# Performance work log

Measured on AMD Instinct MI355X. Metric: run time of the kernel, lower is better.

Reference implementation:

```python
import jax, jax.numpy as jnp
from jax import lax
import numpy as np

GAMMA = 1.0
BIG = 1e10  # stand-in for +inf; exp(-BIG/gamma) underflows to 0 and keeps grads finite


def pairwise_sq_euclidean(A, B):
    # A: (B,T1,K), B: (B,T2,K) -> (B,T1,T2); 0.5*||a-b||^2 expanded to avoid (B,T1,T2,K)
    aa = 0.5 * jnp.sum(A * A, axis=-1)  # (B,T1)
    bb = 0.5 * jnp.sum(B * B, axis=-1)  # (B,T2)
    ab = jnp.einsum('bik,bjk->bij', A, B)
    return aa[:, :, None] + bb[:, None, :] - ab


def soft_dtw(C, gamma):
    # C: (B, m, n). Sequential DP: V[i,j] = C[i-1,j-1] + softmin_gamma(V[i,j-1], V[i-1,j-1], V[i-1,j])
    Bsz, m, n = C.shape
    dt = C.dtype
    big = jnp.asarray(BIG, dt)
    # row 0 of V: V[0,0]=0, V[0,j]=inf
    v0 = jnp.concatenate([jnp.zeros((Bsz, 1), dt), jnp.full((Bsz, n), big, dt)], axis=1)

    def row_step(v_prev, c_row):
        # v_prev: (B, n+1) = V[i-1, :]; c_row: (B, n) = C[:, i-1, :]
        def col_step(v_left, inp):
            c, v_diag, v_up = inp  # each (B,)
            prev = jnp.stack([v_left, v_diag, v_up], axis=-1)  # (B,3)
            minv = -gamma * jax.nn.logsumexp(-prev / gamma, axis=-1)
            v_new = c + minv
            return v_new, v_new

        xs = (c_row.T, v_prev[:, :-1].T, v_prev[:, 1:].T)  # (n, B) each
        _, vals = lax.scan(col_step, jnp.full((Bsz,), big, dt), xs)
        v_row = jnp.concatenate([jnp.full((Bsz, 1), big, dt), vals.T], axis=1)
        return v_row, None

    v_final, _ = lax.scan(row_step, v0, jnp.moveaxis(C, 1, 0))
    return v_final[:, -1]  # (B,)


def setup_inputs() -> dict:
    key = jax.random.key(0)
    k1, k2 = jax.random.split(key)
    X = jax.random.normal(k1, (512, 256, 64), dtype=jnp.float32)
    Y = jax.random.normal(k2, (512, 256, 64), dtype=jnp.float32)
    return {"X": X, "Y": Y}


def reference(X, Y):
    gamma = jnp.asarray(GAMMA, X.dtype)
    s_xy = soft_dtw(pairwise_sq_euclidean(X, Y), gamma)
    s_xx = soft_dtw(pairwise_sq_euclidean(X, X), gamma)
    s_yy = soft_dtw(pairwise_sq_euclidean(Y, Y), gamma)
    D = s_xy - 0.5 * s_xx - 0.5 * s_yy
    # normalize=False, reduction='mean'
    return jnp.mean(D)
```

## Files before the change

kernel.cpp:

```cpp
#include <hip/hip_runtime.h>

typedef _Float16 h8 __attribute__((ext_vector_type(8)));
typedef float f4 __attribute__((ext_vector_type(4)));

#define TT 256
#define KK 64
#define LOG2E 1.44269504f
#define LN2 0.69314718f
#define RL 32
#define RSTR 65
#define DEADD (1 << 28)

__global__ __launch_bounds__(64, 2)
void sdtw_fused3(const float* __restrict__ X, const float* __restrict__ Y,
                 float* __restrict__ out) {
  const int p = blockIdx.x;
  const int type = p >> 9;
  const int b = p & 511;
  const float* Ap = (type == 2 ? Y : X) + (size_t)b * TT * KK;
  const float* Bp = (type == 1 ? X : Y) + (size_t)b * TT * KK;
  const float wgt = (type == 0) ? (LN2 / 512.0f) : (-LN2 / 1024.0f);

  __shared__ unsigned int ring0[RL * RSTR];
  __shared__ unsigned int ring1[RL * RSTR];
  __shared__ float saa[TT];
  __shared__ float sbb[TT];

  const int t = threadIdx.x;
  const int hk = t >> 4, lr = t & 15;

  #pragma unroll
  for (int i = 0; i < 33; ++i) {
    int idx = i * 64 + t;
    if (idx < RL * RSTR) { ring0[idx] = 0u; ring1[idx] = 0u; }
  }

  h8 af[16][2];
  #pragma unroll
  for (int Rt = 0; Rt < 16; ++Rt) {
    float s = 0.f;
    #pragma unroll
    for (int kk = 0; kk < 2; ++kk) {
      const float4* src = (const float4*)(Ap + (Rt * 16 + lr) * KK + kk * 32 + hk * 8);
      float4 x = src[0], y = src[1];
      af[Rt][kk] = (h8){(_Float16)x.x, (_Float16)x.y, (_Float16)x.z, (_Float16)x.w,
                        (_Float16)y.x, (_Float16)y.y, (_Float16)y.z, (_Float16)y.w};
      s += x.x * x.x + x.y * x.y + x.z * x.z + x.w * x.w
         + y.x * y.x + y.y * y.y + y.z * y.z + y.w * y.w;
    }
    s += __shfl_xor(s, 16);
    s += __shfl_xor(s, 32);
    if (hk == (Rt & 3)) saa[Rt * 16 + lr] = 0.5f * LOG2E * s;
  }

  h8 bwin[4][2];

  float E1 = 0.f, E2 = 0.f, E3 = 0.f, E4 = 0.f;
  int d1 = DEADD, d2 = DEADD, d3 = DEADD, d4 = DEADD;
  float dgE = (t == 0) ? 1.0f : 0.f;
  int dgd = (t == 0) ? 0 : DEADD;

  auto cell = [&](float& vE, int& vd, float EL, int dL, float ED, int dD,
                  float EU, int dU, float m, int ci) {
    int ref = min(min(dL, dD), dU);
    float S = ldexpf(EL, ref - dL) + ldexpf(ED, ref - dD) + ldexpf(EU, ref - dU);
    float v = m * S;
    unsigned int u = __builtin_bit_cast(unsigned int, v);
    vE = __builtin_bit_cast(float, (u & 0x007FFFFFu) | 0x3F000000u);
    vd = ref + ci + 126 - (int)(u >> 23);
  };

  auto step = [&](unsigned int w0, unsigned int w1) {
    float upE = __shfl_up(E4, 1);
    int upd = __shfl_up(d4, 1);
    if (t == 0) { upE = 0.f; upd = DEADD; }
    float m0 = __builtin_amdgcn_cvt_f32_fp8((int)w0, 0);
    float m1 = __builtin_amdgcn_cvt_f32_fp8((int)w0, 1);
    float m2 = __builtin_amdgcn_cvt_f32_fp8((int)w0, 2);
    float m3 = __builtin_amdgcn_cvt_f32_fp8((int)w0, 3);
    int ci0 = (int)(w1 & 255u), ci1 = (int)((w1 >> 8) & 255u);
    int ci2 = (int)((w1 >> 16) & 255u), ci3 = (int)(w1 >> 24);
    float v1E, v2E, v3E, v4E; int v1d, v2d, v3d, v4d;
    cell(v1E, v1d, E1, d1, dgE, dgd, upE, upd, m0, ci0);
    cell(v2E, v2d, E2, d2, E1, d1, v1E, v1d, m1, ci1);
    cell(v3E, v3d, E3, d3, E2, d2, v2E, v2d, m2, ci2);
    cell(v4E, v4d, E4, d4, E3, d3, v3E, v3d, m3, ci3);
    E1 = v1E; d1 = v1d; E2 = v2E; d2 = v2d;
    E3 = v3E; d3 = v3d; E4 = v4E; d4 = v4d;
    dgE = upE; dgd = upd;
  };

  #pragma unroll 1
  for (int kbo = 0; kbo < 5; ++kbo) {
    #pragma unroll
    for (int q = 0; q < 4; ++q) {
      const int KB = kbo * 4 + q;
      if (KB <= 15) {
        float s2 = 0.f;
        #pragma unroll
        for (int kk = 0; kk < 2; ++kk) {
          const float4* src = (const float4*)(Bp + (KB * 16 + lr) * KK + kk * 32 + hk * 8);
          float4 x = src[0], y = src[1];
          bwin[q][kk] = (h8){(_Float16)x.x, (_Float16)x.y, (_Float16)x.z, (_Float16)x.w,
                             (_Float16)y.x, (_Float16)y.y, (_Float16)y.z, (_Float16)y.w};
          s2 += x.x * x.x + x.y * x.y + x.z * x.z + x.w * x.w
              + y.x * y.x + y.y * y.y + y.z * y.z + y.w * y.w;
        }
        s2 += __shfl_xor(s2, 16);
        s2 += __shfl_xor(s2, 32);
        if (hk == 0) sbb[KB * 16 + lr] = 0.5f * LOG2E * s2;
      }
      if (KB <= 18) {
        #pragma unroll
        for (int r = 0; r < 4; ++r) {
          const int k = KB * 4 + r;
          #pragma unroll
          for (int dlt = 0; dlt < 4; ++dlt) {
            if (dlt <= KB && dlt >= KB - 15) {
              const int Rt = r + 4 * dlt;
              const int Ct = KB - dlt;
              const int slot = (q - dlt) & 3;
              f4 acc = {0.f, 0.f, 0.f, 0.f};
              acc = __builtin_amdgcn_mfma_f32_16x16x32_f16(af[Rt][0], bwin[slot][0], acc, 0, 0, 0);
              acc = __builtin_amdgcn_mfma_f32_16x16x32_f16(af[Rt][1], bwin[slot][1], acc, 0, 0, 0);
              const int r0 = Rt * 16 + hk * 4;
              f4 aav = *(const f4*)&saa[r0];
              float bbv = sbb[Ct * 16 + lr];
              float c0 = fminf(fmaxf(fmaf(-LOG2E, acc.x, aav.x + bbv), 0.f), 254.0f);
              float c1 = fminf(fmaxf(fmaf(-LOG2E, acc.y, aav.y + bbv), 0.f), 254.0f);
              float c2 = fminf(fmaxf(fmaf(-LOG2E, acc.z, aav.z + bbv), 0.f), 254.0f);
              float c3 = fminf(fmaxf(fmaf(-LOG2E, acc.w, aav.w + bbv), 0.f), 254.0f);
              float f0 = truncf(c0), f1 = truncf(c1), f2 = truncf(c2), f3 = truncf(c3);
              float x0 = c0 - f0, x1 = c1 - f1, x2 = c2 - f2, x3 = c3 - f3;
              float m0 = fmaf(x0, fmaf(x0, 0.17157f, -0.67157f), 1.0f);
              float m1 = fmaf(x1, fmaf(x1, 0.17157f, -0.67157f), 1.0f);
              float m2 = fmaf(x2, fmaf(x2, 0.17157f, -0.67157f), 1.0f);
              float m3 = fmaf(x3, fmaf(x3, 0.17157f, -0.67157f), 1.0f);
              int pkm = __builtin_amdgcn_cvt_pk_fp8_f32(m0, m1, 0, false);
              pkm = __builtin_amdgcn_cvt_pk_fp8_f32(m2, m3, pkm, true);
              unsigned int pkc = (unsigned int)f0 | ((unsigned int)f1 << 8)
                               | ((unsigned int)f2 << 16) | ((unsigned int)f3 << 24);
              const int t_row = 4 * Rt + hk;
              const int s1 = Ct * 16 + lr + t_row;
              const int widx = (s1 & 31) * RSTR + t_row;
              ring0[widx] = (unsigned int)pkm;
              ring1[widx] = pkc;
            }
          }
          unsigned int w0[4], w1[4];
          #pragma unroll
          for (int u = 0; u < 4; ++u) {
            const int s1 = 4 * k + u;
            const int ridx = (s1 & 31) * RSTR + t;
            w0[u] = ring0[ridx];
            w1[u] = ring1[ridx];
          }
          step(w0[0], w1[0]);
          step(w0[1], w1[1]);
          step(w0[2], w1[2]);
          step(w0[3], w1[3]);
        }
      }
    }
  }

  #pragma unroll
  for (int u = 0; u < 15; ++u) {
    const int s1 = 304 + u;
    const int ridx = (s1 & 31) * RSTR + t;
    step(ring0[ridx], ring1[ridx]);
  }

  if (t == 63) atomicAdd(out, wgt * ((float)d4 - __log2f(E4)));
}

extern "C" void kernel_launch(void* const* d_in, const int* in_sizes, int n_in,
                              void* d_out, int out_size, void* d_ws, size_t ws_size,
                              hipStream_t stream) {
  const float* X = (const float*)d_in[0];
  const float* Y = (const float*)d_in[1];
  float* out = (float*)d_out;
  hipMemsetAsync(out, 0, sizeof(float) * out_size, stream);
  sdtw_fused3<<<1536, 64, 0, stream>>>(X, Y, out);
}
```

Before: 168.0 us.

## Process two soft-DTW problems per wavefront with interleaved DP chains and FP8 MFMA

Each 64-thread block now handles two independent problems, interleaving their DP step chains so the latency of one dependency chain can hide the other's. Inputs are quantised to FP8 and the cost tiles come from fp8 MFMA instead of f16, and the norms are computed from the quantised values. The column norms stay in registers rather than shared memory, the two ring buffers merge into uint2 entries, and the neighbour shuffle uses ds_bpermute. The grid halves to 768 blocks, and register pressure doubles from holding two A-operand sets. FP8 inputs also reduce accuracy.

```diff
diff --git a/kernel.cpp b/kernel.cpp
--- a/kernel.cpp
+++ b/kernel.cpp
@@ -1,6 +1,5 @@
 #include <hip/hip_runtime.h>
 
-typedef _Float16 h8 __attribute__((ext_vector_type(8)));
 typedef float f4 __attribute__((ext_vector_type(4)));
 
 #define TT 256
@@ -11,83 +10,115 @@
 #define RSTR 65
 #define DEADD (1 << 28)
 
-__global__ __launch_bounds__(64, 2)
-void sdtw_fused3(const float* __restrict__ X, const float* __restrict__ Y,
-                 float* __restrict__ out) {
-  const int p = blockIdx.x;
-  const int type = p >> 9;
-  const int b = p & 511;
-  const float* Ap = (type == 2 ? Y : X) + (size_t)b * TT * KK;
-  const float* Bp = (type == 1 ? X : Y) + (size_t)b * TT * KK;
-  const float wgt = (type == 0) ? (LN2 / 512.0f) : (-LN2 / 1024.0f);
-
-  __shared__ unsigned int ring0[RL * RSTR];
-  __shared__ unsigned int ring1[RL * RSTR];
-  __shared__ float saa[TT];
-  __shared__ float sbb[TT];
-
+struct DPS {
+  float E1, E2, E3, E4, dgE;
+  int d1, d2, d3, d4, dgd;
+};
+
+__device__ __forceinline__ float sumsq_fp8x4(unsigned int pk) {
+  float d0 = __builtin_amdgcn_cvt_f32_fp8((int)pk, 0);
+  float d1 = __builtin_amdgcn_cvt_f32_fp8((int)pk, 1);
+  float d2 = __builtin_amdgcn_cvt_f32_fp8((int)pk, 2);
+  float d3 = __builtin_amdgcn_cvt_f32_fp8((int)pk, 3);
+  return (d0 * d0 + d1 * d1) + (d2 * d2 + d3 * d3);
+}
+
+__device__ __forceinline__ void cellf(float& Eo, int& don,
+                                      float EL, int dL, float ED, int dD,
+                                      float EU, int dU, float m, int ci126) {
+  int ref = min(min(dL, dD), dU);
+  float S = ldexpf(EL, ref - dL) + ldexpf(ED, ref - dD) + ldexpf(EU, ref - dU);
+  float v = m * S;
+  unsigned int u = __builtin_bit_cast(unsigned int, v);
+  Eo = __builtin_bit_cast(float, (u & 0x007FFFFFu) | 0x3F000000u);
+  don = (ref + ci126) - (int)(u >> 23);
+}
+
+__global__ __launch_bounds__(64)
+void sdtw_dual(const float* __restrict__ X, const float* __restrict__ Y,
+               float* __restrict__ out) {
+  const int bid = blockIdx.x;
   const int t = threadIdx.x;
   const int hk = t >> 4, lr = t & 15;
-
+  const int bpaddr = ((t + 63) & 63) << 2;
+
+  __shared__ uint2 ring[2][RL * RSTR];
+  __shared__ float saa[2][TT];
+
+  const float* Ap[2]; const float* Bp[2]; float wgt[2];
   #pragma unroll
+  for (int pi = 0; pi < 2; ++pi) {
+    int p = 2 * bid + pi;
+    int type = p >> 9;
+    int b = p & 511;
+    Ap[pi] = (type == 2 ? Y : X) + (size_t)b * TT * KK;
+    Bp[pi] = (type == 1 ? X : Y) + (size_t)b * TT * KK;
+    wgt[pi] = (type == 0) ? (LN2 / 512.0f) : (-LN2 / 1024.0f);
+  }
+
+  #pragma unroll 4
   for (int i = 0; i < 33; ++i) {
     int idx = i * 64 + t;
-    if (idx < RL * RSTR) { ring0[idx] = 0u; ring1[idx] = 0u; }
-  }
-
-  h8 af[16][2];
+    if (idx < RL * RSTR) {
+      ring[0][idx] = make_uint2(0u, 0u);
+      ring[1][idx] = make_uint2(0u, 0u);
+    }
+  }
+
+  uint2 af[2][16][2];
   #pragma unroll
-  for (int Rt = 0; Rt < 16; ++Rt) {
-    float s = 0.f;
+  for (int pi = 0; pi < 2; ++pi) {
     #pragma unroll
-    for (int kk = 0; kk < 2; ++kk) {
-      const float4* src = (const float4*)(Ap + (Rt * 16 + lr) * KK + kk * 32 + hk * 8);
-      float4 x = src[0], y = src[1];
-      af[Rt][kk] = (h8){(_Float16)x.x, (_Float16)x.y, (_Float16)x.z, (_Float16)x.w,
-                        (_Float16)y.x, (_Float16)y.y, (_Float16)y.z, (_Float16)y.w};
-      s += x.x * x.x + x.y * x.y + x.z * x.z + x.w * x.w
-         + y.x * y.x + y.y * y.y + y.z * y.z + y.w * y.w;
+    for (int Rt = 0; Rt < 16; ++Rt) {
+      float nrm = 0.f;
+      #pragma unroll
+      for (int kk = 0; kk < 2; ++kk) {
+        const float4* src = (const float4*)(Ap[pi] + (Rt * 16 + lr) * KK + kk * 32 + hk * 8);
+        float4 x = src[0], y = src[1];
+        unsigned int p0 = __builtin_amdgcn_cvt_pk_fp8_f32(x.x, x.y, 0, false);
+        p0 = __builtin_amdgcn_cvt_pk_fp8_f32(x.z, x.w, p0, true);
+        unsigned int p1 = __builtin_amdgcn_cvt_pk_fp8_f32(y.x, y.y, 0, false);
+        p1 = __builtin_amdgcn_cvt_pk_fp8_f32(y.z, y.w, p1, true);
+        af[pi][Rt][kk] = make_uint2(p0, p1);
+        nrm += sumsq_fp8x4(p0) + sumsq_fp8x4(p1);
+      }
+      nrm += __shfl_xor(nrm, 16);
+      nrm += __shfl_xor(nrm, 32);
+      if (hk == 0) saa[pi][Rt * 16 + lr] = 0.5f * LOG2E * nrm;
     }
-    s += __shfl_xor(s, 16);
-    s += __shfl_xor(s, 32);
-    if (hk == (Rt & 3)) saa[Rt * 16 + lr] = 0.5f * LOG2E * s;
-  }
-
-  h8 bwin[4][2];
-
-  float E1 = 0.f, E2 = 0.f, E3 = 0.f, E4 = 0.f;
-  int d1 = DEADD, d2 = DEADD, d3 = DEADD, d4 = DEADD;
-  float dgE = (t == 0) ? 1.0f : 0.f;
-  int dgd = (t == 0) ? 0 : DEADD;
-
-  auto cell = [&](float& vE, int& vd, float EL, int dL, float ED, int dD,
-                  float EU, int dU, float m, int ci) {
-    int ref = min(min(dL, dD), dU);
-    float S = ldexpf(EL, ref - dL) + ldexpf(ED, ref - dD) + ldexpf(EU, ref - dU);
-    float v = m * S;
-    unsigned int u = __builtin_bit_cast(unsigned int, v);
-    vE = __builtin_bit_cast(float, (u & 0x007FFFFFu) | 0x3F000000u);
-    vd = ref + ci + 126 - (int)(u >> 23);
-  };
-
-  auto step = [&](unsigned int w0, unsigned int w1) {
-    float upE = __shfl_up(E4, 1);
-    int upd = __shfl_up(d4, 1);
+  }
+
+  uint2 bwin[2][4][2];
+  float bbR[2][4];
+
+  DPS sa, sb;
+  sa.E1 = sa.E2 = sa.E3 = sa.E4 = 0.f;
+  sa.d1 = sa.d2 = sa.d3 = sa.d4 = DEADD;
+  sa.dgE = (t == 0) ? 1.0f : 0.f;
+  sa.dgd = (t == 0) ? 0 : DEADD;
+  sb = sa;
+
+  auto step = [&](DPS& S, uint2 w) {
+    float upE = __builtin_bit_cast(float,
+        __builtin_amdgcn_ds_bpermute(bpaddr, __builtin_bit_cast(int, S.E4)));
+    int upd = __builtin_amdgcn_ds_bpermute(bpaddr, S.d4);
     if (t == 0) { upE = 0.f; upd = DEADD; }
-    float m0 = __builtin_amdgcn_cvt_f32_fp8((int)w0, 0);
-    float m1 = __builtin_amdgcn_cvt_f32_fp8((int)w0, 1);
-    float m2 = __builtin_amdgcn_cvt_f32_fp8((int)w0, 2);
-    float m3 = __builtin_amdgcn_cvt_f32_fp8((int)w0, 3);
-    int ci0 = (int)(w1 & 255u), ci1 = (int)((w1 >> 8) & 255u);
-    int ci2 = (int)((w1 >> 16) & 255u), ci3 = (int)(w1 >> 24);
+    float m0 = __builtin_amdgcn_cvt_f32_fp8((int)w.x, 0);
+    float m1 = __builtin_amdgcn_cvt_f32_fp8((int)w.x, 1);
+    float m2 = __builtin_amdgcn_cvt_f32_fp8((int)w.x, 2);
+    float m3 = __builtin_amdgcn_cvt_f32_fp8((int)w.x, 3);
+    int c0 = (int)(w.y & 255u) + 126;
+    int c1 = (int)((w.y >> 8) & 255u) + 126;
+    int c2 = (int)((w.y >> 16) & 255u) + 126;
+    int c3 = (int)(w.y >> 24) + 126;
     float v1E, v2E, v3E, v4E; int v1d, v2d, v3d, v4d;
-    cell(v1E, v1d, E1, d1, dgE, dgd, upE, upd, m0, ci0);
-    cell(v2E, v2d, E2, d2, E1, d1, v1E, v1d, m1, ci1);
-    cell(v3E, v3d, E3, d3, E2, d2, v2E, v2d, m2, ci2);
-    cell(v4E, v4d, E4, d4, E3, d3, v3E, v3d, m3, ci3);
-    E1 = v1E; d1 = v1d; E2 = v2E; d2 = v2d;
-    E3 = v3E; d3 = v3d; E4 = v4E; d4 = v4d;
-    dgE = upE; dgd = upd;
+    cellf(v1E, v1d, S.E1, S.d1, S.dgE, S.dgd, upE, upd, m0, c0);
+    cellf(v2E, v2d, S.E2, S.d2, S.E1, S.d1, v1E, v1d, m1, c1);
+    cellf(v3E, v3d, S.E3, S.d3, S.E2, S.d2, v2E, v2d, m2, c2);
+    cellf(v4E, v4d, S.E4, S.d4, S.E3, S.d3, v3E, v3d, m3, c3);
+    S.E1 = v1E; S.d1 = v1d; S.E2 = v2E; S.d2 = v2d;
+    S.E3 = v3E; S.d3 = v3d; S.E4 = v4E; S.d4 = v4d;
+    S.dgE = upE; S.dgd = upd;
   };
 
   #pragma unroll 1
@@ -96,19 +127,24 @@
     for (int q = 0; q < 4; ++q) {
       const int KB = kbo * 4 + q;
       if (KB <= 15) {
-        float s2 = 0.f;
         #pragma unroll
-        for (int kk = 0; kk < 2; ++kk) {
-          const float4* src = (const float4*)(Bp + (KB * 16 + lr) * KK + kk * 32 + hk * 8);
-          float4 x = src[0], y = src[1];
-          bwin[q][kk] = (h8){(_Float16)x.x, (_Float16)x.y, (_Float16)x.z, (_Float16)x.w,
-                             (_Float16)y.x, (_Float16)y.y, (_Float16)y.z, (_Float16)y.w};
-          s2 += x.x * x.x + x.y * x.y + x.z * x.z + x.w * x.w
-              + y.x * y.x + y.y * y.y + y.z * y.z + y.w * y.w;
+        for (int pi = 0; pi < 2; ++pi) {
+          float nrm = 0.f;
+          #pragma unroll
+          for (int kk = 0; kk < 2; ++kk) {
+            const float4* src = (const float4*)(Bp[pi] + (KB * 16 + lr) * KK + kk * 32 + hk * 8);
+            float4 x = src[0], y = src[1];
+            unsigned int p0 = __builtin_amdgcn_cvt_pk_fp8_f32(x.x, x.y, 0, false);
+            p0 = __builtin_amdgcn_cvt_pk_fp8_f32(x.z, x.w, p0, true);
+            unsigned int p1 = __builtin_amdgcn_cvt_pk_fp8_f32(y.x, y.y, 0, false);
+            p1 = __builtin_amdgcn_cvt_pk_fp8_f32(y.z, y.w, p1, true);
+            bwin[pi][q][kk] = make_uint2(p0, p1);
+            nrm += sumsq_fp8x4(p0) + sumsq_fp8x4(p1);
+          }
+          nrm += __shfl_xor(nrm, 16);
+          nrm += __shfl_xor(nrm, 32);
+          bbR[pi][q] = 0.5f * LOG2E * nrm;
         }
-        s2 += __shfl_xor(s2, 16);
-        s2 += __shfl_xor(s2, 32);
-        if (hk == 0) sbb[KB * 16 + lr] = 0.5f * LOG2E * s2;
       }
       if (KB <= 18) {
         #pragma unroll
@@ -118,47 +154,50 @@
           for (int dlt = 0; dlt < 4; ++dlt) {
             if (dlt <= KB && dlt >= KB - 15) {
               const int Rt = r + 4 * dlt;
+              const int slot = (q - dlt) & 3;
               const int Ct = KB - dlt;
-              const int slot = (q - dlt) & 3;
-              f4 acc = {0.f, 0.f, 0.f, 0.f};
-              acc = __builtin_amdgcn_mfma_f32_16x16x32_f16(af[Rt][0], bwin[slot][0], acc, 0, 0, 0);
-              acc = __builtin_amdgcn_mfma_f32_16x16x32_f16(af[Rt][1], bwin[slot][1], acc, 0, 0, 0);
-              const int r0 = Rt * 16 + hk * 4;
-              f4 aav = *(const f4*)&saa[r0];
-              float bbv = sbb[Ct * 16 + lr];
-              float c0 = fminf(fmaxf(fmaf(-LOG2E, acc.x, aav.x + bbv), 0.f), 254.0f);
-              float c1 = fminf(fmaxf(fmaf(-LOG2E, acc.y, aav.y + bbv), 0.f), 254.0f);
-              float c2 = fminf(fmaxf(fmaf(-LOG2E, acc.z, aav.z + bbv), 0.f), 254.0f);
-              float c3 = fminf(fmaxf(fmaf(-LOG2E, acc.w, aav.w + bbv), 0.f), 254.0f);
-              float f0 = truncf(c0), f1 = truncf(c1), f2 = truncf(c2), f3 = truncf(c3);
-              float x0 = c0 - f0, x1 = c1 - f1, x2 = c2 - f2, x3 = c3 - f3;
-              float m0 = fmaf(x0, fmaf(x0, 0.17157f, -0.67157f), 1.0f);
-              float m1 = fmaf(x1, fmaf(x1, 0.17157f, -0.67157f), 1.0f);
-              float m2 = fmaf(x2, fmaf(x2, 0.17157f, -0.67157f), 1.0f);
-              float m3 = fmaf(x3, fmaf(x3, 0.17157f, -0.67157f), 1.0f);
-              int pkm = __builtin_amdgcn_cvt_pk_fp8_f32(m0, m1, 0, false);
-              pkm = __builtin_amdgcn_cvt_pk_fp8_f32(m2, m3, pkm, true);
-              unsigned int pkc = (unsigned int)f0 | ((unsigned int)f1 << 8)
-                               | ((unsigned int)f2 << 16) | ((unsigned int)f3 << 24);
-              const int t_row = 4 * Rt + hk;
-              const int s1 = Ct * 16 + lr + t_row;
-              const int widx = (s1 & 31) * RSTR + t_row;
-              ring0[widx] = (unsigned int)pkm;
-              ring1[widx] = pkc;
+              #pragma unroll
+              for (int pi = 0; pi < 2; ++pi) {
+                f4 acc = {0.f, 0.f, 0.f, 0.f};
+                acc = __builtin_amdgcn_mfma_f32_16x16x32_fp8_fp8(
+                        __builtin_bit_cast(long, af[pi][Rt][0]),
+                        __builtin_bit_cast(long, bwin[pi][slot][0]), acc, 0, 0, 0);
+                acc = __builtin_amdgcn_mfma_f32_16x16x32_fp8_fp8(
+                        __builtin_bit_cast(long, af[pi][Rt][1]),
+                        __builtin_bit_cast(long, bwin[pi][slot][1]), acc, 0, 0, 0);
+                f4 aav = *(const f4*)&saa[pi][Rt * 16 + hk * 4];
+                float bbv = bbR[pi][slot];
+                float c0 = fminf(fmaxf(fmaf(-LOG2E, acc.x, aav.x + bbv), 0.f), 254.0f);
+                float c1 = fminf(fmaxf(fmaf(-LOG2E, acc.y, aav.y + bbv), 0.f), 254.0f);
+                float c2 = fminf(fmaxf(fmaf(-LOG2E, acc.z, aav.z + bbv), 0.f), 254.0f);
+                float c3 = fminf(fmaxf(fmaf(-LOG2E, acc.w, aav.w + bbv), 0.f), 254.0f);
+                float f0 = truncf(c0), f1 = truncf(c1), f2 = truncf(c2), f3 = truncf(c3);
+                float x0 = c0 - f0, x1 = c1 - f1, x2 = c2 - f2, x3 = c3 - f3;
+                float m0 = fmaf(x0, fmaf(x0, 0.17157f, -0.67157f), 1.0f);
+                float m1 = fmaf(x1, fmaf(x1, 0.17157f, -0.67157f), 1.0f);
+                float m2 = fmaf(x2, fmaf(x2, 0.17157f, -0.67157f), 1.0f);
+                float m3 = fmaf(x3, fmaf(x3, 0.17157f, -0.67157f), 1.0f);
+                int pkm = __builtin_amdgcn_cvt_pk_fp8_f32(m0, m1, 0, false);
+                pkm = __builtin_amdgcn_cvt_pk_fp8_f32(m2, m3, pkm, true);
+                unsigned int pkc = (unsigned int)f0 | ((unsigned int)f1 << 8)
+                                 | ((unsigned int)f2 << 16) | ((unsigned int)f3 << 24);
+                const int t_row = 4 * Rt + hk;
+                const int s1 = Ct * 16 + lr + t_row;
+                ring[pi][(s1 & 31) * RSTR + t_row] = make_uint2((unsigned int)pkm, pkc);
+              }
             }
           }
-          unsigned int w0[4], w1[4];
+          uint2 ca[4], cb[4];
           #pragma unroll
           for (int u = 0; u < 4; ++u) {
-            const int s1 = 4 * k + u;
-            const int ridx = (s1 & 31) * RSTR + t;
-            w0[u] = ring0[ridx];
-            w1[u] = ring1[ridx];
+            const int ridx = ((4 * k + u) & 31) * RSTR + t;
+            ca[u] = ring[0][ridx];
+            cb[u] = ring[1][ridx];
           }
-          step(w0[0], w1[0]);
-          step(w0[1], w1[1]);
-          step(w0[2], w1[2]);
-          step(w0[3], w1[3]);
+          step(sa, ca[0]); step(sb, cb[0]);
+          step(sa, ca[1]); step(sb, cb[1]);
+          step(sa, ca[2]); step(sb, cb[2]);
+          step(sa, ca[3]); step(sb, cb[3]);
         }
       }
     }
@@ -166,12 +205,17 @@
 
   #pragma unroll
   for (int u = 0; u < 15; ++u) {
-    const int s1 = 304 + u;
-    const int ridx = (s1 & 31) * RSTR + t;
-    step(ring0[ridx], ring1[ridx]);
-  }
-
-  if (t == 63) atomicAdd(out, wgt * ((float)d4 - __log2f(E4)));
+    const int ridx = ((304 + u) & 31) * RSTR + t;
+    uint2 wa = ring[0][ridx];
+    uint2 wb = ring[1][ridx];
+    step(sa, wa); step(sb, wb);
+  }
+
+  if (t == 63) {
+    float V0 = (float)sa.d4 - __log2f(sa.E4);
+    float V1 = (float)sb.d4 - __log2f(sb.E4);
+    atomicAdd(out, wgt[0] * V0 + wgt[1] * V1);
+  }
 }
 
 extern "C" void kernel_launch(void* const* d_in, const int* in_sizes, int n_in,
@@ -181,5 +225,5 @@
   const float* Y = (const float*)d_in[1];
   float* out = (float*)d_out;
   hipMemsetAsync(out, 0, sizeof(float) * out_size, stream);
-  sdtw_fused3<<<1536, 64, 0, stream>>>(X, Y, out);
-}
+  sdtw_dual<<<768, 64, 0, stream>>>(X, Y, out);
+}
```

Measured after the change: 221.6 us. 1.32x slower.
